# Optimization experiments

Hardware: AMD Instinct MI355X
Metric: run time of the kernel (lower is better)

Reference implementation:

```python
import jax, jax.numpy as jnp
import numpy as np

N = 100000
E = 1600000
IN = 128
HEADS = 8
HID = 16  # out_channels // heads
NEG_SLOPE = 0.2


def setup_inputs() -> dict:
    key = jax.random.key(0)
    k1, k2, k3, k4, k5 = jax.random.split(key, 5)
    x = jax.random.normal(k1, (N, IN), dtype=jnp.float32)
    edge_index = jax.random.randint(k2, (2, E), 0, N, dtype=jnp.int32)
    pos = jax.random.uniform(k3, (N,), dtype=jnp.float32)  # positive per-node weights
    W = jax.random.normal(k4, (HEADS * HID, IN), dtype=jnp.float32) * 0.1  # lin.weight
    att = jax.random.normal(k5, (1, HEADS, 2 * HID), dtype=jnp.float32) * 0.1
    return {"x": x, "edge_index": edge_index, "pos": pos, "W": W, "att": att}


def reference(x, edge_index, pos, W, att):
    n = x.shape[0]
    hid = att.shape[-1] // 2
    heads = att.shape[1]
    # linear projection: [N, heads, hid]
    h = (x @ W.T).reshape(n, heads, hid)
    row, col = edge_index[0], edge_index[1]
    # cat([h[row], h[col]], -1) * att -> sum(-1) == h[row].att_l + h[col].att_r
    att_l = att[0, :, :hid]   # [heads, hid]
    att_r = att[0, :, hid:]   # [heads, hid]
    al = jnp.einsum('nhd,hd->nh', h, att_l)  # [N, heads]
    ar = jnp.einsum('nhd,hd->nh', h, att_r)
    alpha = al[row] + ar[col]                # [E, heads]
    alpha = jnp.where(alpha >= 0, alpha, NEG_SLOPE * alpha)  # LeakyReLU
    # softmax_weights: exp, scale by pos[col], normalize by scatter row-sum
    alpha = jnp.exp(alpha) * pos[col][:, None]
    rowsum = jax.ops.segment_sum(alpha, row, num_segments=n)  # [N, heads]
    inv = 1.0 / rowsum + 1e-16
    alpha = alpha * inv[row]
    # weighted scatter-add aggregation
    out = jax.ops.segment_sum(alpha[:, :, None] * h[col], row, num_segments=n)
    return out.reshape(n, heads * hid)  # concat=True
```

## Files before the change

### kernel.cpp

```cpp
#include <hip/hip_runtime.h>
#include <hip/hip_fp16.h>


#define BK    256
#define BSH   8
#define NBMAX 512
#define BCAP  4736
#define EPB   8

typedef _Float16 half8 __attribute__((ext_vector_type(8)));
typedef float    f32x4 __attribute__((ext_vector_type(4)));

__global__ __launch_bounds__(256) void prep_w(
        const float* __restrict__ W, const float* __restrict__ att,
        _Float16* __restrict__ WBh, _Float16* __restrict__ WBl) {
    int i = blockIdx.x * 256 + threadIdx.x;
    if (i >= 4 * 9 * 64 * 8) return;
    const int j    = i & 7;
    const int lane = (i >> 3) & 63;
    const int ctks = i >> 9;
    const int ct   = ctks % 9;
    const int ks   = ctks / 9;
    const int nn   = lane & 15;
    const int kg   = lane >> 4;
    const int k    = ks * 32 + kg * 8 + j;
    float w;
    if (ct < 8) {
        w = W[(ct * 16 + nn) * 128 + k];
    } else {
        const int head = nn & 7;
        const int sel  = nn >> 3;
        float s = 0.f;
        for (int d = 0; d < 16; ++d)
            s += att[head * 32 + sel * 16 + d] * W[(head * 16 + d) * 128 + k];
        w = s;
    }
    const _Float16 hi = (_Float16)w;
    WBh[i] = hi;
    WBl[i] = (_Float16)(w - (float)hi);
}

__global__ __launch_bounds__(256) void node_h(
        const float* __restrict__ x, const _Float16* __restrict__ WBh,
        const _Float16* __restrict__ WBl,
        _Float16* __restrict__ h, float* __restrict__ al,
        _Float16* __restrict__ arh, int n) {
    const int t    = threadIdx.x;
    const int wv   = t >> 6;
    const int lane = t & 63;
    const int m    = lane & 15;
    const int kg   = lane >> 4;
    const int nodeA = blockIdx.x * 64 + wv * 16 + m;
    const bool avalid = nodeA < n;

    f32x4 acc[9];
#pragma unroll
    for (int ct = 0; ct < 9; ++ct) acc[ct] = (f32x4)0.f;

    const half8* bh = (const half8*)WBh;
    const half8* bl = (const half8*)WBl;

#pragma unroll
    for (int ks = 0; ks < 4; ++ks) {
        float xv[8];
        if (avalid) {
            const float4* xp =
                (const float4*)&x[(size_t)nodeA * 128 + ks * 32 + kg * 8];
            *(float4*)&xv[0] = xp[0];
            *(float4*)&xv[4] = xp[1];
        } else {
#pragma unroll
            for (int j = 0; j < 8; ++j) xv[j] = 0.f;
        }
        half8 axh, axl;
#pragma unroll
        for (int j = 0; j < 8; ++j) {
            const _Float16 hi = (_Float16)xv[j];
            axh[j] = hi;
            axl[j] = (_Float16)(xv[j] - (float)hi);
        }
#pragma unroll
        for (int ct = 0; ct < 9; ++ct) {
            const half8 bhv = bh[(ks * 9 + ct) * 64 + lane];
            const half8 blv = bl[(ks * 9 + ct) * 64 + lane];
            acc[ct] = __builtin_amdgcn_mfma_f32_16x16x32_f16(axl, bhv, acc[ct], 0, 0, 0);
            acc[ct] = __builtin_amdgcn_mfma_f32_16x16x32_f16(axh, blv, acc[ct], 0, 0, 0);
            acc[ct] = __builtin_amdgcn_mfma_f32_16x16x32_f16(axh, bhv, acc[ct], 0, 0, 0);
        }
    }

    const int nodeD0 = blockIdx.x * 64 + wv * 16 + kg * 4;
#pragma unroll
    for (int r = 0; r < 4; ++r) {
        const int node = nodeD0 + r;
        if (node < n) {
#pragma unroll
            for (int ct = 0; ct < 8; ++ct)
                h[(size_t)node * 128 + ct * 16 + m] = (_Float16)acc[ct][r];
            if (m < 8) al[node * 8 + m] = acc[8][r];
            else       arh[node * 8 + (m - 8)] = (_Float16)acc[8][r];
        }
    }
}

__global__ __launch_bounds__(512) void bin_edges(
        const int* __restrict__ ei, int* __restrict__ gcur,
        int* __restrict__ bins, int E, int nb) {
    __shared__ int  cnt[NBMAX];
    __shared__ int  basep[NBMAX];
    __shared__ int  lstart[NBMAX];
    __shared__ int2 sorted[512 * EPB];
    const int t    = threadIdx.x;
    const int base = blockIdx.x * (512 * EPB);
    cnt[t] = 0;
    __syncthreads();

    int rr[EPB], off[EPB];
#pragma unroll
    for (int j = 0; j < EPB; ++j) {
        const int e = base + j * 512 + t;
        if (e < E) {
            rr[j]  = ei[e];
            off[j] = atomicAdd(&cnt[rr[j] >> BSH], 1);
        } else rr[j] = -1;
    }
    __syncthreads();
    const int v = cnt[t];
    lstart[t] = v;
    __syncthreads();
    for (int o = 1; o < 512; o <<= 1) {
        const int tmp = (t >= o) ? lstart[t - o] : 0;
        __syncthreads();
        lstart[t] += tmp;
        __syncthreads();
    }
    const int incl = lstart[t];
    __syncthreads();
    lstart[t] = incl - v;
    basep[t]  = (t < nb && v > 0) ? atomicAdd(&gcur[t], v) : 0;
    __syncthreads();

#pragma unroll
    for (int j = 0; j < EPB; ++j) {
        if (rr[j] >= 0) {
            const int e = base + j * 512 + t;
            const int b = rr[j] >> BSH;
            sorted[lstart[b] + off[j]] = make_int2(ei[E + e], rr[j]);
        }
    }
    __syncthreads();

    const int total = lstart[511] + cnt[511];
    for (int i = t; i < total; i += 512) {
        const int2 p = sorted[i];
        const int  b = p.y >> BSH;
        const int  q = basep[b] + i - lstart[b];
        if (q < BCAP)
            bins[(size_t)b * BCAP + q] = p.x | ((p.y & (BK - 1)) << 17);
    }
}

__global__ __launch_bounds__(256) void bucket_fill(
        const int* __restrict__ bins, const int* __restrict__ gcur,
        int2* __restrict__ rowse, int* __restrict__ csr, int n, int nb) {
    __shared__ int sh[BCAP];
    __shared__ int ld[BK], sc[BK], cur[BK];
    const int b = blockIdx.x, t = threadIdx.x;
    int pv = 0;
    for (int i = t; i < b; i += 256) pv += min(gcur[i], BCAP);
    sc[t] = pv;
    __syncthreads();
    for (int o = 128; o > 0; o >>= 1) {
        if (t < o) sc[t] += sc[t + o];
        __syncthreads();
    }
    const int bbase = sc[0];
    __syncthreads();
    ld[t] = 0;
    __syncthreads();
    const int cnt = min(gcur[b], BCAP);
    const int* bp = bins + (size_t)b * BCAP;
    for (int i = t; i < cnt; i += 256) {
        const int v = bp[i];
        sh[i] = v;
        atomicAdd(&ld[((unsigned)v) >> 17], 1);
    }
    __syncthreads();
    const int v = ld[t];
    sc[t] = v;
    __syncthreads();
    for (int o = 1; o < 256; o <<= 1) {
        const int tmp = (t >= o) ? sc[t - o] : 0;
        __syncthreads();
        sc[t] += tmp;
        __syncthreads();
    }
    const int node = b * BK + t;
    const int s0   = sc[t] - v + bbase;
    cur[t] = s0;
    __syncthreads();
    for (int i = t; i < cnt; i += 256) {
        const int vv = sh[i];
        const int q  = atomicAdd(&cur[((unsigned)vv) >> 17], 1);
        csr[q] = vv & 0x1FFFF;
    }
    __syncthreads();
    if (node < n) rowse[node] = make_int2(s0, cur[t]);
}

__global__ __launch_bounds__(256) void row_gather(
        const int* __restrict__ csr, const int2* __restrict__ rowse,
        const float* __restrict__ al, const _Float16* __restrict__ arh,
        const float* __restrict__ pos, const _Float16* __restrict__ h,
        float* __restrict__ out, int n) {
    const int r    = (blockIdx.x * 256 + threadIdx.x) >> 6;
    const int lane = threadIdx.x & 63;
    if (r >= n) return;
    const int2 se = rowse[r];
    const int s = se.x, e = se.y;
    const int sl = lane & 15;
    if (s >= e) {
        if (lane < 16) {
            float4 z = make_float4(0.f, 0.f, 0.f, 0.f);
            *(float4*)&out[(size_t)r * 128 + sl * 8]     = z;
            *(float4*)&out[(size_t)r * 128 + sl * 8 + 4] = z;
        }
        return;
    }
    const int hd  = lane & 7;
    const int es  = lane >> 3;
    const int esA = lane >> 4;
    const float al_h = al[r * 8 + hd];
    float acc[8];
#pragma unroll
    for (int i = 0; i < 8; ++i) acc[i] = 0.f;
    float rs = 0.f;
    for (int j = s; j < e; j += 8) {
        const int  j1 = j + es;
        const bool v1 = j1 < e;
        const int  c1 = csr[v1 ? j1 : s];
        float av = 0.f;
        if (v1) {
            float a = al_h + (float)arh[(size_t)c1 * 8 + hd];
            a  = (a >= 0.f) ? a : 0.2f * a;
            av = __expf(a) * pos[c1];
            rs += av;
        }
        {
            const int  jA = j + esA;
            const int  cA = csr[(jA < e) ? jA : s];
            const float alpha = __shfl(av, esA * 8 + (sl >> 1), 64);
            float4 hv = *(const float4*)&h[(size_t)cA * 128 + sl * 8];
            const __half2* hp = (const __half2*)&hv;
            const float2 f0 = __half22float2(hp[0]);
            const float2 f1 = __half22float2(hp[1]);
            const float2 f2 = __half22float2(hp[2]);
            const float2 f3 = __half22float2(hp[3]);
            acc[0] = fmaf(alpha, f0.x, acc[0]);
            acc[1] = fmaf(alpha, f0.y, acc[1]);
            acc[2] = fmaf(alpha, f1.x, acc[2]);
            acc[3] = fmaf(alpha, f1.y, acc[3]);
            acc[4] = fmaf(alpha, f2.x, acc[4]);
            acc[5] = fmaf(alpha, f2.y, acc[5]);
            acc[6] = fmaf(alpha, f3.x, acc[6]);
            acc[7] = fmaf(alpha, f3.y, acc[7]);
        }
        {
            const int  jB = j + 4 + esA;
            const int  cB = csr[(jB < e) ? jB : s];
            const float alpha = __shfl(av, 32 + esA * 8 + (sl >> 1), 64);
            float4 hv = *(const float4*)&h[(size_t)cB * 128 + sl * 8];
            const __half2* hp = (const __half2*)&hv;
            const float2 f0 = __half22float2(hp[0]);
            const float2 f1 = __half22float2(hp[1]);
            const float2 f2 = __half22float2(hp[2]);
            const float2 f3 = __half22float2(hp[3]);
            acc[0] = fmaf(alpha, f0.x, acc[0]);
            acc[1] = fmaf(alpha, f0.y, acc[1]);
            acc[2] = fmaf(alpha, f1.x, acc[2]);
            acc[3] = fmaf(alpha, f1.y, acc[3]);
            acc[4] = fmaf(alpha, f2.x, acc[4]);
            acc[5] = fmaf(alpha, f2.y, acc[5]);
            acc[6] = fmaf(alpha, f3.x, acc[6]);
            acc[7] = fmaf(alpha, f3.y, acc[7]);
        }
    }
    rs += __shfl_xor(rs, 8, 64);
    rs += __shfl_xor(rs, 16, 64);
    rs += __shfl_xor(rs, 32, 64);
#pragma unroll
    for (int i = 0; i < 8; ++i) {
        acc[i] += __shfl_xor(acc[i], 16, 64);
        acc[i] += __shfl_xor(acc[i], 32, 64);
    }
    const float rsh = __shfl(rs, (lane & 15) >> 1, 64);
    const float sc  = (rsh != 0.f) ? (1.f / rsh + 1e-16f) : 0.f;
    if (lane < 16) {
        float4 o0 = make_float4(acc[0] * sc, acc[1] * sc, acc[2] * sc, acc[3] * sc);
        float4 o1 = make_float4(acc[4] * sc, acc[5] * sc, acc[6] * sc, acc[7] * sc);
        *(float4*)&out[(size_t)r * 128 + sl * 8]     = o0;
        *(float4*)&out[(size_t)r * 128 + sl * 8 + 4] = o1;
    }
}

extern "C" void kernel_launch(void* const* d_in, const int* in_sizes, int n_in,
                              void* d_out, int out_size, void* d_ws, size_t ws_size,
                              hipStream_t stream) {
    const float* x   = nullptr;
    const int*   ei  = nullptr;
    const float* pos = nullptr;
    const float* W   = nullptr;
    const float* att = nullptr;
    int E2 = 0;
    for (int i = 0; i < n_in; ++i) {
        int s = in_sizes[i];
        if      (s == out_size)        x   = (const float*)d_in[i];
        else if (s == out_size / 128)  pos = (const float*)d_in[i];
        else if (s == 16384)           W   = (const float*)d_in[i];
        else if (s == 256)             att = (const float*)d_in[i];
        else { ei = (const int*)d_in[i]; E2 = s; }
    }
    float* out = (float*)d_out;
    const int N_ = out_size / 128;
    const int E_ = E2 / 2;
    const int NB = (N_ + BK - 1) / BK;

    _Float16* h   = (_Float16*)d_ws;
    float*    al  = (float*)(h + (size_t)N_ * 128);
    _Float16* arh = (_Float16*)(al + (size_t)N_ * 8);
    _Float16* WBh = arh + (size_t)N_ * 8;
    _Float16* WBl = WBh + 18432;
    int2* rowse   = (int2*)(WBl + 18432);
    int* gcur     = (int*)(rowse + N_);
    int* csr      = gcur + NBMAX;
    int* bins     = csr + E_;

    hipMemsetAsync(gcur, 0, (size_t)NBMAX * sizeof(int), stream);

    prep_w<<<72, 256, 0, stream>>>(W, att, WBh, WBl);
    node_h<<<(N_ + 63) / 64, 256, 0, stream>>>(x, WBh, WBl, h, al, arh, N_);
    bin_edges<<<(E_ + 512 * EPB - 1) / (512 * EPB), 512, 0, stream>>>(
        ei, gcur, bins, E_, NB);
    bucket_fill<<<NB, 256, 0, stream>>>(bins, gcur, rowse, csr, N_, NB);
    row_gather<<<(N_ * 64 + 255) / 256, 256, 0, stream>>>(
        csr, rowse, al, arh, pos, h, out, N_);
}
```

Before: 252.1 us.

## Merge node projection and edge binning into one launch, unroll gather loop

Measured after the change: 252.2 us. About the same (+0.1%).

```diff
diff --git a/kernel.cpp b/kernel.cpp
--- a/kernel.cpp
+++ b/kernel.cpp
@@ -13,8 +13,12 @@
 
 __global__ __launch_bounds__(256) void prep_w(
         const float* __restrict__ W, const float* __restrict__ att,
-        _Float16* __restrict__ WBh, _Float16* __restrict__ WBl) {
-    int i = blockIdx.x * 256 + threadIdx.x;
+        _Float16* __restrict__ WBh, _Float16* __restrict__ WBl,
+        int* __restrict__ gcur) {
+    const int t = threadIdx.x;
+    if (blockIdx.x == 0)
+        for (int i = t; i < NBMAX; i += 256) gcur[i] = 0;
+    int i = blockIdx.x * 256 + t;
     if (i >= 4 * 9 * 64 * 8) return;
     const int j    = i & 7;
     const int lane = (i >> 3) & 63;
@@ -40,123 +44,125 @@
     WBl[i] = (_Float16)(w - (float)hi);
 }
 
-__global__ __launch_bounds__(256) void node_h(
+__global__ __launch_bounds__(512) void phase1(
         const float* __restrict__ x, const _Float16* __restrict__ WBh,
         const _Float16* __restrict__ WBl,
         _Float16* __restrict__ h, float* __restrict__ al,
-        _Float16* __restrict__ arh, int n) {
-    const int t    = threadIdx.x;
-    const int wv   = t >> 6;
-    const int lane = t & 63;
-    const int m    = lane & 15;
-    const int kg   = lane >> 4;
-    const int nodeA = blockIdx.x * 64 + wv * 16 + m;
-    const bool avalid = nodeA < n;
-
-    f32x4 acc[9];
-#pragma unroll
-    for (int ct = 0; ct < 9; ++ct) acc[ct] = (f32x4)0.f;
-
-    const half8* bh = (const half8*)WBh;
-    const half8* bl = (const half8*)WBl;
-
-#pragma unroll
-    for (int ks = 0; ks < 4; ++ks) {
-        float xv[8];
-        if (avalid) {
-            const float4* xp =
-                (const float4*)&x[(size_t)nodeA * 128 + ks * 32 + kg * 8];
-            *(float4*)&xv[0] = xp[0];
-            *(float4*)&xv[4] = xp[1];
-        } else {
-#pragma unroll
-            for (int j = 0; j < 8; ++j) xv[j] = 0.f;
-        }
-        half8 axh, axl;
-#pragma unroll
-        for (int j = 0; j < 8; ++j) {
-            const _Float16 hi = (_Float16)xv[j];
-            axh[j] = hi;
-            axl[j] = (_Float16)(xv[j] - (float)hi);
-        }
-#pragma unroll
-        for (int ct = 0; ct < 9; ++ct) {
-            const half8 bhv = bh[(ks * 9 + ct) * 64 + lane];
-            const half8 blv = bl[(ks * 9 + ct) * 64 + lane];
-            acc[ct] = __builtin_amdgcn_mfma_f32_16x16x32_f16(axl, bhv, acc[ct], 0, 0, 0);
-            acc[ct] = __builtin_amdgcn_mfma_f32_16x16x32_f16(axh, blv, acc[ct], 0, 0, 0);
-            acc[ct] = __builtin_amdgcn_mfma_f32_16x16x32_f16(axh, bhv, acc[ct], 0, 0, 0);
-        }
-    }
-
-    const int nodeD0 = blockIdx.x * 64 + wv * 16 + kg * 4;
-#pragma unroll
-    for (int r = 0; r < 4; ++r) {
-        const int node = nodeD0 + r;
-        if (node < n) {
-#pragma unroll
-            for (int ct = 0; ct < 8; ++ct)
-                h[(size_t)node * 128 + ct * 16 + m] = (_Float16)acc[ct][r];
-            if (m < 8) al[node * 8 + m] = acc[8][r];
-            else       arh[node * 8 + (m - 8)] = (_Float16)acc[8][r];
-        }
-    }
-}
-
-__global__ __launch_bounds__(512) void bin_edges(
+        _Float16* __restrict__ arh,
         const int* __restrict__ ei, int* __restrict__ gcur,
-        int* __restrict__ bins, int E, int nb) {
+        int* __restrict__ bins, int n, int E, int nb, int nhBlocks) {
     __shared__ int  cnt[NBMAX];
     __shared__ int  basep[NBMAX];
     __shared__ int  lstart[NBMAX];
     __shared__ int2 sorted[512 * EPB];
-    const int t    = threadIdx.x;
-    const int base = blockIdx.x * (512 * EPB);
-    cnt[t] = 0;
-    __syncthreads();
-
-    int rr[EPB], off[EPB];
-#pragma unroll
-    for (int j = 0; j < EPB; ++j) {
-        const int e = base + j * 512 + t;
-        if (e < E) {
-            rr[j]  = ei[e];
-            off[j] = atomicAdd(&cnt[rr[j] >> BSH], 1);
-        } else rr[j] = -1;
-    }
-    __syncthreads();
-    const int v = cnt[t];
-    lstart[t] = v;
-    __syncthreads();
-    for (int o = 1; o < 512; o <<= 1) {
-        const int tmp = (t >= o) ? lstart[t - o] : 0;
-        __syncthreads();
-        lstart[t] += tmp;
-        __syncthreads();
-    }
-    const int incl = lstart[t];
-    __syncthreads();
-    lstart[t] = incl - v;
-    basep[t]  = (t < nb && v > 0) ? atomicAdd(&gcur[t], v) : 0;
-    __syncthreads();
-
-#pragma unroll
-    for (int j = 0; j < EPB; ++j) {
-        if (rr[j] >= 0) {
+    const int t = threadIdx.x;
+
+    if ((int)blockIdx.x < nhBlocks) {
+        const int blk  = blockIdx.x;
+        const int wv   = t >> 6;
+        const int lane = t & 63;
+        const int m    = lane & 15;
+        const int kg   = lane >> 4;
+        const int nodeA = blk * 128 + wv * 16 + m;
+        const bool avalid = nodeA < n;
+
+        f32x4 acc[9];
+#pragma unroll
+        for (int ct = 0; ct < 9; ++ct) acc[ct] = (f32x4)0.f;
+
+        const half8* bh = (const half8*)WBh;
+        const half8* bl = (const half8*)WBl;
+
+#pragma unroll
+        for (int ks = 0; ks < 4; ++ks) {
+            float xv[8];
+            if (avalid) {
+                const float4* xp =
+                    (const float4*)&x[(size_t)nodeA * 128 + ks * 32 + kg * 8];
+                *(float4*)&xv[0] = xp[0];
+                *(float4*)&xv[4] = xp[1];
+            } else {
+#pragma unroll
+                for (int j = 0; j < 8; ++j) xv[j] = 0.f;
+            }
+            half8 axh, axl;
+#pragma unroll
+            for (int j = 0; j < 8; ++j) {
+                const _Float16 hi = (_Float16)xv[j];
+                axh[j] = hi;
+                axl[j] = (_Float16)(xv[j] - (float)hi);
+            }
+#pragma unroll
+            for (int ct = 0; ct < 9; ++ct) {
+                const half8 bhv = bh[(ks * 9 + ct) * 64 + lane];
+                const half8 blv = bl[(ks * 9 + ct) * 64 + lane];
+                acc[ct] = __builtin_amdgcn_mfma_f32_16x16x32_f16(axl, bhv, acc[ct], 0, 0, 0);
+                acc[ct] = __builtin_amdgcn_mfma_f32_16x16x32_f16(axh, blv, acc[ct], 0, 0, 0);
+                acc[ct] = __builtin_amdgcn_mfma_f32_16x16x32_f16(axh, bhv, acc[ct], 0, 0, 0);
+            }
+        }
+
+        const int nodeD0 = blk * 128 + wv * 16 + kg * 4;
+#pragma unroll
+        for (int r = 0; r < 4; ++r) {
+            const int node = nodeD0 + r;
+            if (node < n) {
+#pragma unroll
+                for (int ct = 0; ct < 8; ++ct)
+                    h[(size_t)node * 128 + ct * 16 + m] = (_Float16)acc[ct][r];
+                if (m < 8) al[node * 8 + m] = acc[8][r];
+                else       arh[node * 8 + (m - 8)] = (_Float16)acc[8][r];
+            }
+        }
+    } else {
+        const int blk  = blockIdx.x - nhBlocks;
+        const int base = blk * (512 * EPB);
+        cnt[t] = 0;
+        __syncthreads();
+
+        int rr[EPB], off[EPB];
+#pragma unroll
+        for (int j = 0; j < EPB; ++j) {
             const int e = base + j * 512 + t;
-            const int b = rr[j] >> BSH;
-            sorted[lstart[b] + off[j]] = make_int2(ei[E + e], rr[j]);
-        }
-    }
-    __syncthreads();
-
-    const int total = lstart[511] + cnt[511];
-    for (int i = t; i < total; i += 512) {
-        const int2 p = sorted[i];
-        const int  b = p.y >> BSH;
-        const int  q = basep[b] + i - lstart[b];
-        if (q < BCAP)
-            bins[(size_t)b * BCAP + q] = p.x | ((p.y & (BK - 1)) << 17);
+            if (e < E) {
+                rr[j]  = ei[e];
+                off[j] = atomicAdd(&cnt[rr[j] >> BSH], 1);
+            } else rr[j] = -1;
+        }
+        __syncthreads();
+        const int v = cnt[t];
+        lstart[t] = v;
+        __syncthreads();
+        for (int o = 1; o < 512; o <<= 1) {
+            const int tmp = (t >= o) ? lstart[t - o] : 0;
+            __syncthreads();
+            lstart[t] += tmp;
+            __syncthreads();
+        }
+        const int incl = lstart[t];
+        __syncthreads();
+        lstart[t] = incl - v;
+        basep[t]  = (t < nb && v > 0) ? atomicAdd(&gcur[t], v) : 0;
+        __syncthreads();
+
+#pragma unroll
+        for (int j = 0; j < EPB; ++j) {
+            if (rr[j] >= 0) {
+                const int e = base + j * 512 + t;
+                const int b = rr[j] >> BSH;
+                sorted[lstart[b] + off[j]] = make_int2(ei[E + e], rr[j]);
+            }
+        }
+        __syncthreads();
+
+        const int total = lstart[511] + cnt[511];
+        for (int i = t; i < total; i += 512) {
+            const int2 p = sorted[i];
+            const int  b = p.y >> BSH;
+            const int  q = basep[b] + i - lstart[b];
+            if (q < BCAP)
+                bins[(size_t)b * BCAP + q] = p.x | ((p.y & (BK - 1)) << 17);
+        }
     }
 }
 
@@ -230,59 +236,72 @@
     const int hd  = lane & 7;
     const int es  = lane >> 3;
     const int esA = lane >> 4;
+    const int src = (sl >> 1);
     const float al_h = al[r * 8 + hd];
     float acc[8];
 #pragma unroll
     for (int i = 0; i < 8; ++i) acc[i] = 0.f;
     float rs = 0.f;
-    for (int j = s; j < e; j += 8) {
-        const int  j1 = j + es;
-        const bool v1 = j1 < e;
-        const int  c1 = csr[v1 ? j1 : s];
-        float av = 0.f;
-        if (v1) {
-            float a = al_h + (float)arh[(size_t)c1 * 8 + hd];
-            a  = (a >= 0.f) ? a : 0.2f * a;
-            av = __expf(a) * pos[c1];
-            rs += av;
-        }
+    for (int j = s; j < e; j += 16) {
+        float av0 = 0.f;
+        {
+            const int  j1 = j + es;
+            const bool v1 = j1 < e;
+            const int  c1 = csr[v1 ? j1 : s];
+            if (v1) {
+                float a = al_h + (float)arh[(size_t)c1 * 8 + hd];
+                a   = (a >= 0.f) ? a : 0.2f * a;
+                av0 = __expf(a) * pos[c1];
+            }
+        }
+        float av1 = 0.f;
+        const bool have2 = (j + 8) < e;
+        if (have2) {
+            const int  j2 = j + 8 + es;
+            const bool v2 = j2 < e;
+            const int  c2 = csr[v2 ? j2 : s];
+            if (v2) {
+                float a = al_h + (float)arh[(size_t)c2 * 8 + hd];
+                a   = (a >= 0.f) ? a : 0.2f * a;
+                av1 = __expf(a) * pos[c2];
+            }
+        }
+        rs += av0 + av1;
         {
             const int  jA = j + esA;
             const int  cA = csr[(jA < e) ? jA : s];
-            const float alpha = __shfl(av, esA * 8 + (sl >> 1), 64);
-            float4 hv = *(const float4*)&h[(size_t)cA * 128 + sl * 8];
-            const __half2* hp = (const __half2*)&hv;
-            const float2 f0 = __half22float2(hp[0]);
-            const float2 f1 = __half22float2(hp[1]);
-            const float2 f2 = __half22float2(hp[2]);
-            const float2 f3 = __half22float2(hp[3]);
-            acc[0] = fmaf(alpha, f0.x, acc[0]);
-            acc[1] = fmaf(alpha, f0.y, acc[1]);
-            acc[2] = fmaf(alpha, f1.x, acc[2]);
-            acc[3] = fmaf(alpha, f1.y, acc[3]);
-            acc[4] = fmaf(alpha, f2.x, acc[4]);
-            acc[5] = fmaf(alpha, f2.y, acc[5]);
-            acc[6] = fmaf(alpha, f3.x, acc[6]);
-            acc[7] = fmaf(alpha, f3.y, acc[7]);
-        }
-        {
+            const float alpha = __shfl(av0, esA * 8 + src, 64);
+            const half8 hv = *(const half8*)&h[(size_t)cA * 128 + sl * 8];
+#pragma unroll
+            for (int i = 0; i < 8; ++i)
+                acc[i] = fmaf(alpha, (float)hv[i], acc[i]);
+        }
+        if (j + 4 < e) {
             const int  jB = j + 4 + esA;
             const int  cB = csr[(jB < e) ? jB : s];
-            const float alpha = __shfl(av, 32 + esA * 8 + (sl >> 1), 64);
-            float4 hv = *(const float4*)&h[(size_t)cB * 128 + sl * 8];
-            const __half2* hp = (const __half2*)&hv;
-            const float2 f0 = __half22float2(hp[0]);
-            const float2 f1 = __half22float2(hp[1]);
-            const float2 f2 = __half22float2(hp[2]);
-            const float2 f3 = __half22float2(hp[3]);
-            acc[0] = fmaf(alpha, f0.x, acc[0]);
-            acc[1] = fmaf(alpha, f0.y, acc[1]);
-            acc[2] = fmaf(alpha, f1.x, acc[2]);
-            acc[3] = fmaf(alpha, f1.y, acc[3]);
-            acc[4] = fmaf(alpha, f2.x, acc[4]);
-            acc[5] = fmaf(alpha, f2.y, acc[5]);
-            acc[6] = fmaf(alpha, f3.x, acc[6]);
-            acc[7] = fmaf(alpha, f3.y, acc[7]);
+            const float alpha = __shfl(av0, 32 + esA * 8 + src, 64);
+            const half8 hv = *(const half8*)&h[(size_t)cB * 128 + sl * 8];
+#pragma unroll
+            for (int i = 0; i < 8; ++i)
+                acc[i] = fmaf(alpha, (float)hv[i], acc[i]);
+        }
+        if (have2) {
+            const int  jC = j + 8 + esA;
+            const int  cC = csr[(jC < e) ? jC : s];
+            const float alpha = __shfl(av1, esA * 8 + src, 64);
+            const half8 hv = *(const half8*)&h[(size_t)cC * 128 + sl * 8];
+#pragma unroll
+            for (int i = 0; i < 8; ++i)
+                acc[i] = fmaf(alpha, (float)hv[i], acc[i]);
+        }
+        if (j + 12 < e) {
+            const int  jD = j + 12 + esA;
+            const int  cD = csr[(jD < e) ? jD : s];
+            const float alpha = __shfl(av1, 32 + esA * 8 + src, 64);
+            const half8 hv = *(const half8*)&h[(size_t)cD * 128 + sl * 8];
+#pragma unroll
+            for (int i = 0; i < 8; ++i)
+                acc[i] = fmaf(alpha, (float)hv[i], acc[i]);
         }
     }
     rs += __shfl_xor(rs, 8, 64);
@@ -293,7 +312,7 @@
         acc[i] += __shfl_xor(acc[i], 16, 64);
         acc[i] += __shfl_xor(acc[i], 32, 64);
     }
-    const float rsh = __shfl(rs, (lane & 15) >> 1, 64);
+    const float rsh = __shfl(rs, src, 64);
     const float sc  = (rsh != 0.f) ? (1.f / rsh + 1e-16f) : 0.f;
     if (lane < 16) {
         float4 o0 = make_float4(acc[0] * sc, acc[1] * sc, acc[2] * sc, acc[3] * sc);
@@ -335,12 +354,12 @@
     int* csr      = gcur + NBMAX;
     int* bins     = csr + E_;
 
-    hipMemsetAsync(gcur, 0, (size_t)NBMAX * sizeof(int), stream);
-
-    prep_w<<<72, 256, 0, stream>>>(W, att, WBh, WBl);
-    node_h<<<(N_ + 63) / 64, 256, 0, stream>>>(x, WBh, WBl, h, al, arh, N_);
-    bin_edges<<<(E_ + 512 * EPB - 1) / (512 * EPB), 512, 0, stream>>>(
-        ei, gcur, bins, E_, NB);
+    const int nhBlocks = (N_ + 127) / 128;
+    const int beBlocks = (E_ + 512 * EPB - 1) / (512 * EPB);
+
+    prep_w<<<72, 256, 0, stream>>>(W, att, WBh, WBl, gcur);
+    phase1<<<nhBlocks + beBlocks, 512, 0, stream>>>(
+        x, WBh, WBl, h, al, arh, ei, gcur, bins, N_, E_, NB, nhBlocks);
     bucket_fill<<<NB, 256, 0, stream>>>(bins, gcur, rowse, csr, N_, NB);
     row_gather<<<(N_ * 64 + 255) / 256, 256, 0, stream>>>(
         csr, rowse, al, arh, pos, h, out, N_);
```

## Fuse node projection with edge binning, and bucket CSR build with row gather

Applied to the files above, without the earlier changes.

New measurement: 229.9 us. 8.8% less time.

```diff
diff --git a/kernel.cpp b/kernel.cpp
--- a/kernel.cpp
+++ b/kernel.cpp
@@ -7,14 +7,19 @@
 #define NBMAX 512
 #define BCAP  4736
 #define EPB   8
+#define GT    1024
 
 typedef _Float16 half8 __attribute__((ext_vector_type(8)));
 typedef float    f32x4 __attribute__((ext_vector_type(4)));
 
 __global__ __launch_bounds__(256) void prep_w(
         const float* __restrict__ W, const float* __restrict__ att,
-        _Float16* __restrict__ WBh, _Float16* __restrict__ WBl) {
-    int i = blockIdx.x * 256 + threadIdx.x;
+        _Float16* __restrict__ WBh, _Float16* __restrict__ WBl,
+        int* __restrict__ gcur) {
+    const int t = threadIdx.x;
+    if (blockIdx.x == 0)
+        for (int i = t; i < NBMAX; i += 256) gcur[i] = 0;
+    int i = blockIdx.x * 256 + t;
     if (i >= 4 * 9 * 64 * 8) return;
     const int j    = i & 7;
     const int lane = (i >> 3) & 63;
@@ -40,266 +45,263 @@
     WBl[i] = (_Float16)(w - (float)hi);
 }
 
-__global__ __launch_bounds__(256) void node_h(
+__global__ __launch_bounds__(512) void phase1(
         const float* __restrict__ x, const _Float16* __restrict__ WBh,
         const _Float16* __restrict__ WBl,
         _Float16* __restrict__ h, float* __restrict__ al,
-        _Float16* __restrict__ arh, int n) {
-    const int t    = threadIdx.x;
-    const int wv   = t >> 6;
-    const int lane = t & 63;
-    const int m    = lane & 15;
-    const int kg   = lane >> 4;
-    const int nodeA = blockIdx.x * 64 + wv * 16 + m;
-    const bool avalid = nodeA < n;
-
-    f32x4 acc[9];
-#pragma unroll
-    for (int ct = 0; ct < 9; ++ct) acc[ct] = (f32x4)0.f;
-
-    const half8* bh = (const half8*)WBh;
-    const half8* bl = (const half8*)WBl;
-
-#pragma unroll
-    for (int ks = 0; ks < 4; ++ks) {
-        float xv[8];
-        if (avalid) {
-            const float4* xp =
-                (const float4*)&x[(size_t)nodeA * 128 + ks * 32 + kg * 8];
-            *(float4*)&xv[0] = xp[0];
-            *(float4*)&xv[4] = xp[1];
-        } else {
-#pragma unroll
-            for (int j = 0; j < 8; ++j) xv[j] = 0.f;
-        }
-        half8 axh, axl;
-#pragma unroll
-        for (int j = 0; j < 8; ++j) {
-            const _Float16 hi = (_Float16)xv[j];
-            axh[j] = hi;
-            axl[j] = (_Float16)(xv[j] - (float)hi);
-        }
-#pragma unroll
-        for (int ct = 0; ct < 9; ++ct) {
-            const half8 bhv = bh[(ks * 9 + ct) * 64 + lane];
-            const half8 blv = bl[(ks * 9 + ct) * 64 + lane];
-            acc[ct] = __builtin_amdgcn_mfma_f32_16x16x32_f16(axl, bhv, acc[ct], 0, 0, 0);
-            acc[ct] = __builtin_amdgcn_mfma_f32_16x16x32_f16(axh, blv, acc[ct], 0, 0, 0);
-            acc[ct] = __builtin_amdgcn_mfma_f32_16x16x32_f16(axh, bhv, acc[ct], 0, 0, 0);
-        }
-    }
-
-    const int nodeD0 = blockIdx.x * 64 + wv * 16 + kg * 4;
-#pragma unroll
-    for (int r = 0; r < 4; ++r) {
-        const int node = nodeD0 + r;
-        if (node < n) {
-#pragma unroll
-            for (int ct = 0; ct < 8; ++ct)
-                h[(size_t)node * 128 + ct * 16 + m] = (_Float16)acc[ct][r];
-            if (m < 8) al[node * 8 + m] = acc[8][r];
-            else       arh[node * 8 + (m - 8)] = (_Float16)acc[8][r];
-        }
-    }
-}
-
-__global__ __launch_bounds__(512) void bin_edges(
+        _Float16* __restrict__ arh,
         const int* __restrict__ ei, int* __restrict__ gcur,
-        int* __restrict__ bins, int E, int nb) {
+        int* __restrict__ bins, int n, int E, int nb, int nhBlocks) {
     __shared__ int  cnt[NBMAX];
     __shared__ int  basep[NBMAX];
     __shared__ int  lstart[NBMAX];
     __shared__ int2 sorted[512 * EPB];
-    const int t    = threadIdx.x;
-    const int base = blockIdx.x * (512 * EPB);
-    cnt[t] = 0;
-    __syncthreads();
-
-    int rr[EPB], off[EPB];
-#pragma unroll
-    for (int j = 0; j < EPB; ++j) {
-        const int e = base + j * 512 + t;
-        if (e < E) {
-            rr[j]  = ei[e];
-            off[j] = atomicAdd(&cnt[rr[j] >> BSH], 1);
-        } else rr[j] = -1;
-    }
-    __syncthreads();
-    const int v = cnt[t];
-    lstart[t] = v;
-    __syncthreads();
-    for (int o = 1; o < 512; o <<= 1) {
-        const int tmp = (t >= o) ? lstart[t - o] : 0;
-        __syncthreads();
-        lstart[t] += tmp;
-        __syncthreads();
-    }
-    const int incl = lstart[t];
-    __syncthreads();
-    lstart[t] = incl - v;
-    basep[t]  = (t < nb && v > 0) ? atomicAdd(&gcur[t], v) : 0;
-    __syncthreads();
-
-#pragma unroll
-    for (int j = 0; j < EPB; ++j) {
-        if (rr[j] >= 0) {
+    const int t = threadIdx.x;
+
+    if ((int)blockIdx.x < nhBlocks) {
+        const int blk  = blockIdx.x;
+        const int wv   = t >> 6;
+        const int lane = t & 63;
+        const int m    = lane & 15;
+        const int kg   = lane >> 4;
+        const int nodeA = blk * 128 + wv * 16 + m;
+        const bool avalid = nodeA < n;
+
+        f32x4 acc[9];
+#pragma unroll
+        for (int ct = 0; ct < 9; ++ct) acc[ct] = (f32x4)0.f;
+
+        const half8* bh = (const half8*)WBh;
+        const half8* bl = (const half8*)WBl;
+
+#pragma unroll
+        for (int ks = 0; ks < 4; ++ks) {
+            float xv[8];
+            if (avalid) {
+                const float4* xp =
+                    (const float4*)&x[(size_t)nodeA * 128 + ks * 32 + kg * 8];
+                *(float4*)&xv[0] = xp[0];
+                *(float4*)&xv[4] = xp[1];
+            } else {
+#pragma unroll
+                for (int j = 0; j < 8; ++j) xv[j] = 0.f;
+            }
+            half8 axh, axl;
+#pragma unroll
+            for (int j = 0; j < 8; ++j) {
+                const _Float16 hi = (_Float16)xv[j];
+                axh[j] = hi;
+                axl[j] = (_Float16)(xv[j] - (float)hi);
+            }
+#pragma unroll
+            for (int ct = 0; ct < 9; ++ct) {
+                const half8 bhv = bh[(ks * 9 + ct) * 64 + lane];
+                const half8 blv = bl[(ks * 9 + ct) * 64 + lane];
+                acc[ct] = __builtin_amdgcn_mfma_f32_16x16x32_f16(axl, bhv, acc[ct], 0, 0, 0);
+                acc[ct] = __builtin_amdgcn_mfma_f32_16x16x32_f16(axh, blv, acc[ct], 0, 0, 0);
+                acc[ct] = __builtin_amdgcn_mfma_f32_16x16x32_f16(axh, bhv, acc[ct], 0, 0, 0);
+            }
+        }
+
+        const int nodeD0 = blk * 128 + wv * 16 + kg * 4;
+#pragma unroll
+        for (int r = 0; r < 4; ++r) {
+            const int node = nodeD0 + r;
+            if (node < n) {
+#pragma unroll
+                for (int ct = 0; ct < 8; ++ct)
+                    h[(size_t)node * 128 + ct * 16 + m] = (_Float16)acc[ct][r];
+                if (m < 8) al[node * 8 + m] = acc[8][r];
+                else       arh[node * 8 + (m - 8)] = (_Float16)acc[8][r];
+            }
+        }
+    } else {
+        const int blk  = blockIdx.x - nhBlocks;
+        const int base = blk * (512 * EPB);
+        cnt[t] = 0;
+        __syncthreads();
+
+        int rr[EPB], off[EPB];
+#pragma unroll
+        for (int j = 0; j < EPB; ++j) {
             const int e = base + j * 512 + t;
-            const int b = rr[j] >> BSH;
-            sorted[lstart[b] + off[j]] = make_int2(ei[E + e], rr[j]);
-        }
-    }
-    __syncthreads();
-
-    const int total = lstart[511] + cnt[511];
-    for (int i = t; i < total; i += 512) {
-        const int2 p = sorted[i];
-        const int  b = p.y >> BSH;
-        const int  q = basep[b] + i - lstart[b];
-        if (q < BCAP)
-            bins[(size_t)b * BCAP + q] = p.x | ((p.y & (BK - 1)) << 17);
+            if (e < E) {
+                rr[j]  = ei[e];
+                off[j] = atomicAdd(&cnt[rr[j] >> BSH], 1);
+            } else rr[j] = -1;
+        }
+        __syncthreads();
+        const int v = cnt[t];
+        lstart[t] = v;
+        __syncthreads();
+        for (int o = 1; o < 512; o <<= 1) {
+            const int tmp = (t >= o) ? lstart[t - o] : 0;
+            __syncthreads();
+            lstart[t] += tmp;
+            __syncthreads();
+        }
+        const int incl = lstart[t];
+        __syncthreads();
+        lstart[t] = incl - v;
+        basep[t]  = (t < nb && v > 0) ? atomicAdd(&gcur[t], v) : 0;
+        __syncthreads();
+
+#pragma unroll
+        for (int j = 0; j < EPB; ++j) {
+            if (rr[j] >= 0) {
+                const int e = base + j * 512 + t;
+                const int b = rr[j] >> BSH;
+                sorted[lstart[b] + off[j]] = make_int2(ei[E + e], rr[j]);
+            }
+        }
+        __syncthreads();
+
+        const int total = lstart[511] + cnt[511];
+        for (int i = t; i < total; i += 512) {
+            const int2 p = sorted[i];
+            const int  b = p.y >> BSH;
+            const int  q = basep[b] + i - lstart[b];
+            if (q < BCAP)
+                bins[(size_t)b * BCAP + q] = p.x | ((p.y & (BK - 1)) << 17);
+        }
     }
 }
 
-__global__ __launch_bounds__(256) void bucket_fill(
+__global__ __launch_bounds__(GT) void bucket_gather(
         const int* __restrict__ bins, const int* __restrict__ gcur,
-        int2* __restrict__ rowse, int* __restrict__ csr, int n, int nb) {
-    __shared__ int sh[BCAP];
-    __shared__ int ld[BK], sc[BK], cur[BK];
-    const int b = blockIdx.x, t = threadIdx.x;
-    int pv = 0;
-    for (int i = t; i < b; i += 256) pv += min(gcur[i], BCAP);
-    sc[t] = pv;
-    __syncthreads();
-    for (int o = 128; o > 0; o >>= 1) {
-        if (t < o) sc[t] += sc[t + o];
-        __syncthreads();
-    }
-    const int bbase = sc[0];
-    __syncthreads();
-    ld[t] = 0;
-    __syncthreads();
-    const int cnt = min(gcur[b], BCAP);
-    const int* bp = bins + (size_t)b * BCAP;
-    for (int i = t; i < cnt; i += 256) {
-        const int v = bp[i];
-        sh[i] = v;
-        atomicAdd(&ld[((unsigned)v) >> 17], 1);
-    }
-    __syncthreads();
-    const int v = ld[t];
-    sc[t] = v;
-    __syncthreads();
-    for (int o = 1; o < 256; o <<= 1) {
-        const int tmp = (t >= o) ? sc[t - o] : 0;
-        __syncthreads();
-        sc[t] += tmp;
-        __syncthreads();
-    }
-    const int node = b * BK + t;
-    const int s0   = sc[t] - v + bbase;
-    cur[t] = s0;
-    __syncthreads();
-    for (int i = t; i < cnt; i += 256) {
-        const int vv = sh[i];
-        const int q  = atomicAdd(&cur[((unsigned)vv) >> 17], 1);
-        csr[q] = vv & 0x1FFFF;
-    }
-    __syncthreads();
-    if (node < n) rowse[node] = make_int2(s0, cur[t]);
-}
-
-__global__ __launch_bounds__(256) void row_gather(
-        const int* __restrict__ csr, const int2* __restrict__ rowse,
         const float* __restrict__ al, const _Float16* __restrict__ arh,
         const float* __restrict__ pos, const _Float16* __restrict__ h,
         float* __restrict__ out, int n) {
-    const int r    = (blockIdx.x * 256 + threadIdx.x) >> 6;
-    const int lane = threadIdx.x & 63;
-    if (r >= n) return;
-    const int2 se = rowse[r];
-    const int s = se.x, e = se.y;
-    const int sl = lane & 15;
-    if (s >= e) {
+    __shared__ int sh[BCAP];
+    __shared__ int csrL[BCAP];
+    __shared__ int rstart[BK], sc[BK], cur[BK];
+    const int b = blockIdx.x, t = threadIdx.x;
+    if (t < BK) rstart[t] = 0;
+    __syncthreads();
+    const int cnt = min(gcur[b], BCAP);
+    const int* bp = bins + (size_t)b * BCAP;
+    for (int i = t; i < cnt; i += GT) {
+        const int v = bp[i];
+        sh[i] = v;
+        atomicAdd(&rstart[((unsigned)v) >> 17], 1);
+    }
+    __syncthreads();
+    if (t < BK) sc[t] = rstart[t];
+    __syncthreads();
+    for (int o = 1; o < BK; o <<= 1) {
+        int tmp = 0;
+        if (t < BK && t >= o) tmp = sc[t - o];
+        __syncthreads();
+        if (t < BK) sc[t] += tmp;
+        __syncthreads();
+    }
+    if (t < BK) {
+        const int v  = rstart[t];
+        const int s0 = sc[t] - v;
+        rstart[t] = s0;
+        cur[t]    = s0;
+    }
+    __syncthreads();
+    for (int i = t; i < cnt; i += GT) {
+        const int vv = sh[i];
+        const int q  = atomicAdd(&cur[((unsigned)vv) >> 17], 1);
+        csrL[q] = vv & 0x1FFFF;
+    }
+    __syncthreads();
+
+    const int wv   = t >> 6;
+    const int lane = t & 63;
+    const int sl   = lane & 15;
+    const int hd   = lane & 7;
+    const int es   = lane >> 3;
+    const int esA  = lane >> 4;
+    const int src  = sl >> 1;
+    for (int rr = wv; rr < BK; rr += 16) {
+        const int r = b * BK + rr;
+        if (r >= n) break;
+        const int s = rstart[rr];
+        const int e = cur[rr];
+        if (s >= e) {
+            if (lane < 16) {
+                float4 z = make_float4(0.f, 0.f, 0.f, 0.f);
+                *(float4*)&out[(size_t)r * 128 + sl * 8]     = z;
+                *(float4*)&out[(size_t)r * 128 + sl * 8 + 4] = z;
+            }
+            continue;
+        }
+        const float al_h = al[r * 8 + hd];
+        float acc[8];
+#pragma unroll
+        for (int i = 0; i < 8; ++i) acc[i] = 0.f;
+        float rs = 0.f;
+        for (int j = s; j < e; j += 8) {
+            const int  j1 = j + es;
+            const bool v1 = j1 < e;
+            const int  c1 = csrL[v1 ? j1 : s];
+            float av = 0.f;
+            if (v1) {
+                float a = al_h + (float)arh[(size_t)c1 * 8 + hd];
+                a  = (a >= 0.f) ? a : 0.2f * a;
+                av = __expf(a) * pos[c1];
+                rs += av;
+            }
+            {
+                const int  jA = j + esA;
+                const int  cA = csrL[(jA < e) ? jA : s];
+                const float alpha = __shfl(av, esA * 8 + src, 64);
+                float4 hv = *(const float4*)&h[(size_t)cA * 128 + sl * 8];
+                const __half2* hp = (const __half2*)&hv;
+                const float2 f0 = __half22float2(hp[0]);
+                const float2 f1 = __half22float2(hp[1]);
+                const float2 f2 = __half22float2(hp[2]);
+                const float2 f3 = __half22float2(hp[3]);
+                acc[0] = fmaf(alpha, f0.x, acc[0]);
+                acc[1] = fmaf(alpha, f0.y, acc[1]);
+                acc[2] = fmaf(alpha, f1.x, acc[2]);
+                acc[3] = fmaf(alpha, f1.y, acc[3]);
+                acc[4] = fmaf(alpha, f2.x, acc[4]);
+                acc[5] = fmaf(alpha, f2.y, acc[5]);
+                acc[6] = fmaf(alpha, f3.x, acc[6]);
+                acc[7] = fmaf(alpha, f3.y, acc[7]);
+            }
+            {
+                const int  jB = j + 4 + esA;
+                const int  cB = csrL[(jB < e) ? jB : s];
+                const float alpha = __shfl(av, 32 + esA * 8 + src, 64);
+                float4 hv = *(const float4*)&h[(size_t)cB * 128 + sl * 8];
+                const __half2* hp = (const __half2*)&hv;
+                const float2 f0 = __half22float2(hp[0]);
+                const float2 f1 = __half22float2(hp[1]);
+                const float2 f2 = __half22float2(hp[2]);
+                const float2 f3 = __half22float2(hp[3]);
+                acc[0] = fmaf(alpha, f0.x, acc[0]);
+                acc[1] = fmaf(alpha, f0.y, acc[1]);
+                acc[2] = fmaf(alpha, f1.x, acc[2]);
+                acc[3] = fmaf(alpha, f1.y, acc[3]);
+                acc[4] = fmaf(alpha, f2.x, acc[4]);
+                acc[5] = fmaf(alpha, f2.y, acc[5]);
+                acc[6] = fmaf(alpha, f3.x, acc[6]);
+                acc[7] = fmaf(alpha, f3.y, acc[7]);
+            }
+        }
+        rs += __shfl_xor(rs, 8, 64);
+        rs += __shfl_xor(rs, 16, 64);
+        rs += __shfl_xor(rs, 32, 64);
+#pragma unroll
+        for (int i = 0; i < 8; ++i) {
+            acc[i] += __shfl_xor(acc[i], 16, 64);
+            acc[i] += __shfl_xor(acc[i], 32, 64);
+        }
+        const float rsh = __shfl(rs, src, 64);
+        const float scl = (rsh != 0.f) ? (1.f / rsh + 1e-16f) : 0.f;
         if (lane < 16) {
-            float4 z = make_float4(0.f, 0.f, 0.f, 0.f);
-            *(float4*)&out[(size_t)r * 128 + sl * 8]     = z;
-            *(float4*)&out[(size_t)r * 128 + sl * 8 + 4] = z;
-        }
-        return;
-    }
-    const int hd  = lane & 7;
-    const int es  = lane >> 3;
-    const int esA = lane >> 4;
-    const float al_h = al[r * 8 + hd];
-    float acc[8];
-#pragma unroll
-    for (int i = 0; i < 8; ++i) acc[i] = 0.f;
-    float rs = 0.f;
-    for (int j = s; j < e; j += 8) {
-        const int  j1 = j + es;
-        const bool v1 = j1 < e;
-        const int  c1 = csr[v1 ? j1 : s];
-        float av = 0.f;
-        if (v1) {
-            float a = al_h + (float)arh[(size_t)c1 * 8 + hd];
-            a  = (a >= 0.f) ? a : 0.2f * a;
-            av = __expf(a) * pos[c1];
-            rs += av;
-        }
-        {
-            const int  jA = j + esA;
-            const int  cA = csr[(jA < e) ? jA : s];
-            const float alpha = __shfl(av, esA * 8 + (sl >> 1), 64);
-            float4 hv = *(const float4*)&h[(size_t)cA * 128 + sl * 8];
-            const __half2* hp = (const __half2*)&hv;
-            const float2 f0 = __half22float2(hp[0]);
-            const float2 f1 = __half22float2(hp[1]);
-            const float2 f2 = __half22float2(hp[2]);
-            const float2 f3 = __half22float2(hp[3]);
-            acc[0] = fmaf(alpha, f0.x, acc[0]);
-            acc[1] = fmaf(alpha, f0.y, acc[1]);
-            acc[2] = fmaf(alpha, f1.x, acc[2]);
-            acc[3] = fmaf(alpha, f1.y, acc[3]);
-            acc[4] = fmaf(alpha, f2.x, acc[4]);
-            acc[5] = fmaf(alpha, f2.y, acc[5]);
-            acc[6] = fmaf(alpha, f3.x, acc[6]);
-            acc[7] = fmaf(alpha, f3.y, acc[7]);
-        }
-        {
-            const int  jB = j + 4 + esA;
-            const int  cB = csr[(jB < e) ? jB : s];
-            const float alpha = __shfl(av, 32 + esA * 8 + (sl >> 1), 64);
-            float4 hv = *(const float4*)&h[(size_t)cB * 128 + sl * 8];
-            const __half2* hp = (const __half2*)&hv;
-            const float2 f0 = __half22float2(hp[0]);
-            const float2 f1 = __half22float2(hp[1]);
-            const float2 f2 = __half22float2(hp[2]);
-            const float2 f3 = __half22float2(hp[3]);
-            acc[0] = fmaf(alpha, f0.x, acc[0]);
-            acc[1] = fmaf(alpha, f0.y, acc[1]);
-            acc[2] = fmaf(alpha, f1.x, acc[2]);
-            acc[3] = fmaf(alpha, f1.y, acc[3]);
-            acc[4] = fmaf(alpha, f2.x, acc[4]);
-            acc[5] = fmaf(alpha, f2.y, acc[5]);
-            acc[6] = fmaf(alpha, f3.x, acc[6]);
-            acc[7] = fmaf(alpha, f3.y, acc[7]);
-        }
-    }
-    rs += __shfl_xor(rs, 8, 64);
-    rs += __shfl_xor(rs, 16, 64);
-    rs += __shfl_xor(rs, 32, 64);
-#pragma unroll
-    for (int i = 0; i < 8; ++i) {
-        acc[i] += __shfl_xor(acc[i], 16, 64);
-        acc[i] += __shfl_xor(acc[i], 32, 64);
-    }
-    const float rsh = __shfl(rs, (lane & 15) >> 1, 64);
-    const float sc  = (rsh != 0.f) ? (1.f / rsh + 1e-16f) : 0.f;
-    if (lane < 16) {
-        float4 o0 = make_float4(acc[0] * sc, acc[1] * sc, acc[2] * sc, acc[3] * sc);
-        float4 o1 = make_float4(acc[4] * sc, acc[5] * sc, acc[6] * sc, acc[7] * sc);
-        *(float4*)&out[(size_t)r * 128 + sl * 8]     = o0;
-        *(float4*)&out[(size_t)r * 128 + sl * 8 + 4] = o1;
+            float4 o0 = make_float4(acc[0] * scl, acc[1] * scl,
+                                    acc[2] * scl, acc[3] * scl);
+            float4 o1 = make_float4(acc[4] * scl, acc[5] * scl,
+                                    acc[6] * scl, acc[7] * scl);
+            *(float4*)&out[(size_t)r * 128 + sl * 8]     = o0;
+            *(float4*)&out[(size_t)r * 128 + sl * 8 + 4] = o1;
+        }
     }
 }
 
@@ -330,18 +332,14 @@
     _Float16* arh = (_Float16*)(al + (size_t)N_ * 8);
     _Float16* WBh = arh + (size_t)N_ * 8;
     _Float16* WBl = WBh + 18432;
-    int2* rowse   = (int2*)(WBl + 18432);
-    int* gcur     = (int*)(rowse + N_);
-    int* csr      = gcur + NBMAX;
-    int* bins     = csr + E_;
-
-    hipMemsetAsync(gcur, 0, (size_t)NBMAX * sizeof(int), stream);
-
-    prep_w<<<72, 256, 0, stream>>>(W, att, WBh, WBl);
-    node_h<<<(N_ + 63) / 64, 256, 0, stream>>>(x, WBh, WBl, h, al, arh, N_);
-    bin_edges<<<(E_ + 512 * EPB - 1) / (512 * EPB), 512, 0, stream>>>(
-        ei, gcur, bins, E_, NB);
-    bucket_fill<<<NB, 256, 0, stream>>>(bins, gcur, rowse, csr, N_, NB);
-    row_gather<<<(N_ * 64 + 255) / 256, 256, 0, stream>>>(
-        csr, rowse, al, arh, pos, h, out, N_);
+    int* gcur     = (int*)(WBl + 18432);
+    int* bins     = gcur + NBMAX;
+
+    const int nhBlocks = (N_ + 127) / 128;
+    const int beBlocks = (E_ + 512 * EPB - 1) / (512 * EPB);
+
+    prep_w<<<72, 256, 0, stream>>>(W, att, WBh, WBl, gcur);
+    phase1<<<nhBlocks + beBlocks, 512, 0, stream>>>(
+        x, WBh, WBl, h, al, arh, ei, gcur, bins, N_, E_, NB, nhBlocks);
+    bucket_gather<<<NB, GT, 0, stream>>>(bins, gcur, al, arh, pos, h, out, N_);
 }
```
